# Kernel tuning notes

Measured on AMD Instinct MI355X. Metric: run time of the kernel, lower is better.

## Reference

```python
import jax, jax.numpy as jnp
import numpy as np

PS = 32
D = 256


def setup_inputs() -> dict:
    key = jax.random.key(0)
    ks = jax.random.split(key, 9)
    B, L = 32, 32768
    s_in = 1.0 / np.sqrt(PS)
    s_d = 1.0 / np.sqrt(D)
    return {
        "x": jax.random.normal(ks[0], (B, L), dtype=jnp.float32),
        "W_proj": jax.random.normal(ks[1], (PS, D), dtype=jnp.float32) * s_in,
        "b_proj": jnp.zeros((D,), jnp.float32),
        "W_qkv": jax.random.normal(ks[2], (D, 3 * D), dtype=jnp.float32) * s_d,
        "b_qkv": jnp.zeros((3 * D,), jnp.float32),
        "W_out": jax.random.normal(ks[3], (D, D), dtype=jnp.float32) * s_d,
        "b_out": jnp.zeros((D,), jnp.float32),
        "W_head": jax.random.normal(ks[4], (D, PS), dtype=jnp.float32) * s_d,
        "b_head": jnp.zeros((PS,), jnp.float32),
    }


def reference(x, W_proj, b_proj, W_qkv, b_qkv, W_out, b_out, W_head, b_head):
    B, L = x.shape
    T = L // PS
    # InstanceNorm over full series (torch .std is unbiased -> ddof=1)
    mean = jnp.mean(x, axis=-1, keepdims=True)
    std = jnp.std(x, axis=-1, keepdims=True, ddof=1) + 1e-5
    x_norm = (x - mean) / std
    patches = x_norm.reshape(B, T, PS)
    # Patch embedding
    h = patches @ W_proj + b_proj  # [B, T, D]
    # Single-head causal self-attention (explicit scores, as in source)
    qkv = h @ W_qkv + b_qkv
    q, k, v = jnp.split(qkv, 3, axis=-1)
    scale = 1.0 / jnp.sqrt(jnp.asarray(D, dtype=h.dtype))
    attn = jnp.einsum("btd,bsd->bts", q, k) * scale  # [B, T, T]
    causal = jnp.tril(jnp.ones((T, T), dtype=bool))
    attn = jnp.where(causal, attn, -jnp.inf)
    attn = jax.nn.softmax(attn, axis=-1)
    out = jnp.einsum("bts,bsd->btd", attn, v)
    out = out @ W_out + b_out
    # Prediction head + next-patch MSE loss
    pred = out @ W_head + b_head  # [B, T, PS]
    loss = jnp.mean((pred[:, :-1] - patches[:, 1:]) ** 2)
    return loss
```

## Files before the change

kernel.cpp:

```cpp
#include <hip/hip_runtime.h>
#include <math.h>

#define B_SZ 32
#define L_SZ 32768
#define T_SZ 1024
#define PS_SZ 32
#define D_SZ 256
#define SM_M 10.0f

typedef float f32x4 __attribute__((ext_vector_type(4)));
typedef float f32x16 __attribute__((ext_vector_type(16)));
typedef short s16x8 __attribute__((ext_vector_type(8)));
typedef unsigned short u16x8 __attribute__((ext_vector_type(8)));

__device__ __forceinline__ unsigned short f2bf(float f) {
  union { float f; unsigned int u; } v; v.f = f;
  unsigned int r = v.u + 0x7FFFu + ((v.u >> 16) & 1u);
  return (unsigned short)(r >> 16);
}

__device__ __forceinline__ void g2l16(const unsigned short* g, unsigned short* l) {
  __builtin_amdgcn_global_load_lds(
      (const __attribute__((address_space(1))) unsigned int*)g,
      (__attribute__((address_space(3))) unsigned int*)l, 16, 0, 0);
}

__global__ __launch_bounds__(256) void prep_kernel(const float* __restrict__ x,
                                                   float* __restrict__ sgpart,
                                                   const float* __restrict__ Wp,
                                                   const float* __restrict__ bp,
                                                   const float* __restrict__ Wq,
                                                   const float* __restrict__ bq,
                                                   const float* __restrict__ Wo,
                                                   const float* __restrict__ bo,
                                                   const float* __restrict__ Wh,
                                                   const float* __restrict__ bh,
                                                   float* __restrict__ Wcb,
                                                   unsigned short* __restrict__ WqT,
                                                   unsigned short* __restrict__ WfT,
                                                   float* __restrict__ bfp,
                                                   unsigned int* __restrict__ total,
                                                   float* __restrict__ lsum) {
  __shared__ float red[8];
  const int g = blockIdx.x, tid = threadIdx.x;
  const int w = tid >> 6, lane = tid & 63;
  if (g < 256) {
    const int b = g >> 3;
    const float* p = x + (size_t)b * L_SZ + (size_t)(g & 7) * 4096;
    float s = 0.f, ss = 0.f;
#pragma unroll
    for (int i = 0; i < 4; ++i) {
      float4 f = ((const float4*)p)[tid + i * 256];
      s += f.x + f.y + f.z + f.w;
      ss += f.x * f.x + f.y * f.y + f.z * f.z + f.w * f.w;
    }
#pragma unroll
    for (int off = 32; off >= 1; off >>= 1) {
      s += __shfl_down(s, off);
      ss += __shfl_down(ss, off);
    }
    if (lane == 0) { red[w] = s; red[4 + w] = ss; }
    __syncthreads();
    if (tid == 0) {
      sgpart[g * 2]     = red[0] + red[1] + red[2] + red[3];
      sgpart[g * 2 + 1] = red[4] + red[5] + red[6] + red[7];
    }
  } else if (g < 388) {
    int idx = (g - 256) * 256 + tid;
    if (idx < 33 * 768) {
      int p = idx / 768, j = idx % 768;
      const float* arow = (p < 32) ? (Wp + p * 256) : bp;
      float acc = (p < 32) ? 0.f : bq[j];
      for (int d = 0; d < 256; ++d) acc += arow[d] * Wq[d * 768 + j];
      if (p < 32) WqT[j * 32 + p] = f2bf(acc);
      else Wcb[j] = acc;
    } else {
      int k = idx - 33 * 768;
      if (k < 8192) {
        int p = k >> 8, d = k & 255;
        float acc = 0.f;
        for (int e = 0; e < 256; ++e) acc += Wo[d * 256 + e] * Wh[e * 32 + p];
        WfT[p * 256 + d] = f2bf(acc);
      } else if (k < 8224) {
        int p = k - 8192;
        float acc = bh[p];
        for (int e = 0; e < 256; ++e) acc += bo[e] * Wh[e * 32 + p];
        bfp[p] = acc;
      }
    }
  } else {
    if (tid == 0) { total[0] = 0u; lsum[0] = 0.f; }
  }
}

__global__ __launch_bounds__(256) void qkv_kernel(const float* __restrict__ x,
                                                  const float* __restrict__ sgpart,
                                                  const unsigned short* __restrict__ WqT,
                                                  const float* __restrict__ Wcb,
                                                  unsigned short* __restrict__ Qb,
                                                  unsigned short* __restrict__ Kb,
                                                  unsigned short* __restrict__ Vtt) {
  __shared__ unsigned short T4[4][8448];
  const int tid = threadIdx.x;
  const int w = tid >> 6, lane = tid & 63;
  const int lo = lane & 15, quad = lane >> 4;
  unsigned short* Tw = T4[w];
  const int mbase = blockIdx.x * 128 + w * 32;
  const int b = mbase >> 10;
  float S = 0.f, SS = 0.f;
#pragma unroll
  for (int i = 0; i < 8; ++i) {
    S += sgpart[(b * 8 + i) * 2];
    SS += sgpart[(b * 8 + i) * 2 + 1];
  }
  const float mean = S * (1.f / (float)L_SZ);
  const float var = (SS - S * mean) * (1.f / (float)(L_SZ - 1));
  const float inv = 1.f / (sqrtf(var) + 1e-5f);
  s16x8 af0, af1;
  {
    float4 a = *(const float4*)&x[(size_t)(mbase + lo) * 32 + quad * 8];
    float4 c = *(const float4*)&x[(size_t)(mbase + lo) * 32 + quad * 8 + 4];
    af0[0] = (short)f2bf((a.x - mean) * inv); af0[1] = (short)f2bf((a.y - mean) * inv);
    af0[2] = (short)f2bf((a.z - mean) * inv); af0[3] = (short)f2bf((a.w - mean) * inv);
    af0[4] = (short)f2bf((c.x - mean) * inv); af0[5] = (short)f2bf((c.y - mean) * inv);
    af0[6] = (short)f2bf((c.z - mean) * inv); af0[7] = (short)f2bf((c.w - mean) * inv);
    float4 d = *(const float4*)&x[(size_t)(mbase + 16 + lo) * 32 + quad * 8];
    float4 e = *(const float4*)&x[(size_t)(mbase + 16 + lo) * 32 + quad * 8 + 4];
    af1[0] = (short)f2bf((d.x - mean) * inv); af1[1] = (short)f2bf((d.y - mean) * inv);
    af1[2] = (short)f2bf((d.z - mean) * inv); af1[3] = (short)f2bf((d.w - mean) * inv);
    af1[4] = (short)f2bf((e.x - mean) * inv); af1[5] = (short)f2bf((e.y - mean) * inv);
    af1[6] = (short)f2bf((e.z - mean) * inv); af1[7] = (short)f2bf((e.w - mean) * inv);
  }
#pragma unroll 4
  for (int nt = 0; nt < 16; ++nt) {
    s16x8 bf = *(const s16x8*)&WqT[(size_t)(nt * 16 + lo) * 32 + quad * 8];
    f32x4 c0 = {0.f, 0.f, 0.f, 0.f}, c1 = {0.f, 0.f, 0.f, 0.f};
    c0 = __builtin_amdgcn_mfma_f32_16x16x32_bf16(af0, bf, c0, 0, 0, 0);
    c1 = __builtin_amdgcn_mfma_f32_16x16x32_bf16(af1, bf, c1, 0, 0, 0);
    const int col = nt * 16 + lo;
    const float bi = Wcb[col];
#pragma unroll
    for (int i = 0; i < 4; ++i) {
      Tw[(quad * 4 + i) * 264 + col]      = f2bf((c0[i] + bi) * 0.0625f);
      Tw[(16 + quad * 4 + i) * 264 + col] = f2bf((c1[i] + bi) * 0.0625f);
    }
  }
#pragma unroll
  for (int it = 0; it < 16; ++it) {
    const int gsub = it * 64 + lane;
    const int row = gsub >> 5, c16 = gsub & 31;
    *(u16x8*)&Qb[(size_t)(mbase + row) * 256 + c16 * 8] =
        *(const u16x8*)&Tw[row * 264 + c16 * 8];
  }
#pragma unroll 4
  for (int nt = 0; nt < 16; ++nt) {
    s16x8 bf = *(const s16x8*)&WqT[(size_t)(256 + nt * 16 + lo) * 32 + quad * 8];
    f32x4 c0 = {0.f, 0.f, 0.f, 0.f}, c1 = {0.f, 0.f, 0.f, 0.f};
    c0 = __builtin_amdgcn_mfma_f32_16x16x32_bf16(af0, bf, c0, 0, 0, 0);
    c1 = __builtin_amdgcn_mfma_f32_16x16x32_bf16(af1, bf, c1, 0, 0, 0);
    const int col = nt * 16 + lo;
    const float bi = Wcb[256 + col];
#pragma unroll
    for (int i = 0; i < 4; ++i) {
      Tw[(quad * 4 + i) * 264 + col]      = f2bf(c0[i] + bi);
      Tw[(16 + quad * 4 + i) * 264 + col] = f2bf(c1[i] + bi);
    }
  }
#pragma unroll
  for (int it = 0; it < 16; ++it) {
    const int gsub = it * 64 + lane;
    const int row = gsub >> 5, c16 = gsub & 31;
    *(u16x8*)&Kb[(size_t)(mbase + row) * 256 + c16 * 8] =
        *(const u16x8*)&Tw[row * 264 + c16 * 8];
  }
#pragma unroll 4
  for (int nt2 = 0; nt2 < 16; ++nt2) {
    s16x8 aw = *(const s16x8*)&WqT[(size_t)(512 + nt2 * 16 + lo) * 32 + quad * 8];
    f32x4 c0 = {0.f, 0.f, 0.f, 0.f}, c1 = {0.f, 0.f, 0.f, 0.f};
    c0 = __builtin_amdgcn_mfma_f32_16x16x32_bf16(aw, af0, c0, 0, 0, 0);
    c1 = __builtin_amdgcn_mfma_f32_16x16x32_bf16(aw, af1, c1, 0, 0, 0);
#pragma unroll
    for (int i = 0; i < 4; ++i) {
      const int d = nt2 * 16 + quad * 4 + i;
      const float bv = Wcb[512 + d];
      Tw[d * 32 + lo]      = f2bf(c0[i] + bv);
      Tw[d * 32 + 16 + lo] = f2bf(c1[i] + bv);
    }
  }
  {
    const int ktq = (mbase >> 5) & 31;
    const size_t vb = ((size_t)b * 32 + ktq) * 8192;
#pragma unroll
    for (int it = 0; it < 16; ++it) {
      const int gsub = it * 64 + lane;
      *(u16x8*)&Vtt[vb + gsub * 8] = *(const u16x8*)&Tw[gsub * 8];
    }
  }
}

__global__ __launch_bounds__(128, 1) void attn_kernel(const unsigned short* __restrict__ Qb,
                                                      const unsigned short* __restrict__ Kb,
                                                      const unsigned short* __restrict__ Vtt,
                                                      const unsigned short* __restrict__ WfT,
                                                      const float* __restrict__ bfp,
                                                      const float* __restrict__ x,
                                                      const float* __restrict__ sgpart,
                                                      float* __restrict__ lsum,
                                                      unsigned int* __restrict__ total,
                                                      float* __restrict__ out) {
  __shared__ unsigned short SMEM[36352];
  __shared__ float redf[2];
  __shared__ unsigned int flag;
  const int g = blockIdx.x;
  const int j = g >> 3;
  const int b = (g & 7) * 4 + (j & 3);
  const int qt = (j < 32) ? (15 - (j >> 2)) : ((j - 32) >> 2);
  const int tid = threadIdx.x;
  const int w = tid >> 6, lane = tid & 63;
  const int cl = lane & 31, hi = lane >> 5;
  const int qr0 = qt * 64 + w * 32;

  s16x8 qf[16];
  {
    const size_t qrow = ((size_t)(b * 1024 + qr0 + cl)) * 256;
#pragma unroll
    for (int cb = 0; cb < 16; ++cb)
      qf[cb] = *(const s16x8*)&Qb[qrow + cb * 16 + hi * 8];
  }

  f32x16 O[8], Ol;
#pragma unroll
  for (int dt = 0; dt < 8; ++dt)
#pragma unroll
    for (int i = 0; i < 16; ++i) O[dt][i] = 0.f;
#pragma unroll
  for (int i = 0; i < 16; ++i) Ol[i] = 0.f;
  s16x8 ones;
#pragma unroll
  for (int jj = 0; jj < 8; ++jj) ones[jj] = (short)0x3F80;

  int kof[8];
#pragma unroll
  for (int it = 0; it < 8; ++it) {
    const int key = it * 4 + (tid >> 5);
    kof[it] = key * 256 + ((tid & 31) ^ key) * 8;
  }
  const int vof = (tid >> 2) * 32 + (((tid & 3) ^ ((tid >> 4) & 3))) * 8;
  const unsigned short* KbB = Kb + (size_t)b * 262144;
  const unsigned short* VtB = Vtt + (size_t)b * 262144;
  const int wb = w * 512;
  const int nk = 2 * (qt + 1);

#pragma unroll
  for (int it = 0; it < 8; ++it) g2l16(KbB + kof[it], &SMEM[it * 1024 + wb]);
#pragma unroll
  for (int it = 0; it < 8; ++it) g2l16(VtB + vof + it * 1024, &SMEM[8192 + it * 1024 + wb]);

  const int maskl = (cl >> 2) & 3;
  const int cv0 = (hi ^ maskl) * 8;
  const int cv1 = ((2 | hi) ^ maskl) * 8;
  unsigned short* Pw = &SMEM[32768 + w * 1792];
  const int prow = cl * 56;

  for (int kt = 0; kt < nk; ++kt) {
    const int k0 = kt * 32;
    __syncthreads();
    const int cur = (kt & 1) << 14;
    if (kt + 1 < nk) {
      const int nxt = ((kt + 1) & 1) << 14;
      const int ko = (kt + 1) * 8192;
#pragma unroll
      for (int it = 0; it < 8; ++it) g2l16(KbB + ko + kof[it], &SMEM[nxt + it * 1024 + wb]);
#pragma unroll
      for (int it = 0; it < 8; ++it)
        g2l16(VtB + ko + vof + it * 1024, &SMEM[nxt + 8192 + it * 1024 + wb]);
    }

    if (k0 <= qr0 + 31) {
      f32x16 S;
#pragma unroll
      for (int i = 0; i < 16; ++i) S[i] = 0.f;
      const int kbl = cur + cl * 256;
#pragma unroll
      for (int cb = 0; cb < 16; ++cb) {
        s16x8 kf = *(const s16x8*)&SMEM[kbl + ((((cb << 1) | hi) ^ cl) << 3)];
        S = __builtin_amdgcn_mfma_f32_32x32x16_bf16(qf[cb], kf, S, 0, 0, 0);
      }
      const bool diag = (k0 + 31 > qr0);
#pragma unroll
      for (int r = 0; r < 16; ++r) {
        const int row = (r & 3) + 8 * (r >> 2) + 4 * hi;
        float e = __expf(S[r] - SM_M);
        if (diag && (k0 + cl > qr0 + row)) e = 0.f;
        Pw[row * 56 + cl] = f2bf(e);
      }
      s16x8 pf0 = *(const s16x8*)&Pw[prow + hi * 8];
      s16x8 pf1 = *(const s16x8*)&Pw[prow + 16 + hi * 8];
      Ol = __builtin_amdgcn_mfma_f32_32x32x16_bf16(pf0, ones, Ol, 0, 0, 0);
      Ol = __builtin_amdgcn_mfma_f32_32x32x16_bf16(pf1, ones, Ol, 0, 0, 0);
      const int vbl = cur + 8192 + cl * 32;
#pragma unroll
      for (int dt = 0; dt < 8; ++dt) {
        s16x8 v0 = *(const s16x8*)&SMEM[vbl + dt * 1024 + cv0];
        s16x8 v1 = *(const s16x8*)&SMEM[vbl + dt * 1024 + cv1];
        O[dt] = __builtin_amdgcn_mfma_f32_32x32x16_bf16(pf0, v0, O[dt], 0, 0, 0);
        O[dt] = __builtin_amdgcn_mfma_f32_32x32x16_bf16(pf1, v1, O[dt], 0, 0, 0);
      }
    }
  }
  __syncthreads();

  unsigned short* OLw = &SMEM[w * 8448];
#pragma unroll
  for (int r = 0; r < 16; ++r) {
    const int row = (r & 3) + 8 * (r >> 2) + 4 * hi;
    const float iv = 1.f / Ol[r];
#pragma unroll
    for (int dt = 0; dt < 8; ++dt)
      OLw[row * 264 + dt * 32 + cl] = f2bf(O[dt][r] * iv);
  }
  s16x8 af[16];
#pragma unroll
  for (int cb = 0; cb < 16; ++cb)
    af[cb] = *(const s16x8*)&OLw[cl * 264 + cb * 16 + hi * 8];

  float S_ = 0.f, SS = 0.f;
#pragma unroll
  for (int i = 0; i < 8; ++i) {
    S_ += sgpart[(b * 8 + i) * 2];
    SS += sgpart[(b * 8 + i) * 2 + 1];
  }
  const float mean = S_ * (1.f / (float)L_SZ);
  const float var = (SS - S_ * mean) * (1.f / (float)(L_SZ - 1));
  const float invb = 1.f / (sqrtf(var) + 1e-5f);

  f32x16 hacc;
#pragma unroll
  for (int i = 0; i < 16; ++i) hacc[i] = 0.f;
#pragma unroll
  for (int cb = 0; cb < 16; ++cb) {
    s16x8 bfr = *(const s16x8*)&WfT[(size_t)cl * 256 + cb * 16 + hi * 8];
    hacc = __builtin_amdgcn_mfma_f32_32x32x16_bf16(af[cb], bfr, hacc, 0, 0, 0);
  }
  const float ba = bfp[cl];
  float lacc = 0.f;
#pragma unroll
  for (int r = 0; r < 16; ++r) {
    const int row = (r & 3) + 8 * (r >> 2) + 4 * hi;
    const int t = qr0 + row;
    if (t < 1023) {
      const float pr = hacc[r] + ba;
      const float tg = (x[(size_t)b * L_SZ + (t + 1) * 32 + cl] - mean) * invb;
      const float d = pr - tg;
      lacc += d * d;
    }
  }
#pragma unroll
  for (int off = 32; off >= 1; off >>= 1) lacc += __shfl_down(lacc, off);
  if (lane == 0) redf[w] = lacc;
  __syncthreads();

  if (tid == 0) {
    atomicAdd(lsum, redf[0] + redf[1]);
    __threadfence();
    unsigned int prev = atomicAdd(total, 1u);
    flag = (prev == 511u) ? 1u : 0u;
  }
  __syncthreads();
  if (flag && tid == 0) {
    float tot = atomicAdd(lsum, 0.0f);
    out[0] = tot * (1.f / (float)(B_SZ * (T_SZ - 1) * PS_SZ));
  }
}

extern "C" void kernel_launch(void* const* d_in, const int* in_sizes, int n_in,
                              void* d_out, int out_size, void* d_ws, size_t ws_size,
                              hipStream_t stream) {
  const float* x      = (const float*)d_in[0];
  const float* W_proj = (const float*)d_in[1];
  const float* b_proj = (const float*)d_in[2];
  const float* W_qkv  = (const float*)d_in[3];
  const float* b_qkv  = (const float*)d_in[4];
  const float* W_out  = (const float*)d_in[5];
  const float* b_out  = (const float*)d_in[6];
  const float* W_head = (const float*)d_in[7];
  const float* b_head = (const float*)d_in[8];
  float* out = (float*)d_out;
  char* ws = (char*)d_ws;

  unsigned short* Qb     = (unsigned short*)ws;
  unsigned short* Kb     = (unsigned short*)(ws + (16ull << 20));
  unsigned short* Vtt    = (unsigned short*)(ws + (32ull << 20));
  char* tail = ws + (48ull << 20);
  float*          Wcb    = (float*)tail;
  unsigned short* WqT    = (unsigned short*)(tail + 4096);
  unsigned short* WfT    = (unsigned short*)(tail + 65536);
  float*          bfp    = (float*)(tail + 98304);
  float*          sgpart = (float*)(tail + 102400);
  unsigned int*   total  = (unsigned int*)(tail + 106496);
  float*          lsum   = (float*)(tail + 106496 + 64);

  prep_kernel<<<389, 256, 0, stream>>>(x, sgpart, W_proj, b_proj, W_qkv, b_qkv,
                                       W_out, b_out, W_head, b_head,
                                       Wcb, WqT, WfT, bfp, total, lsum);
  qkv_kernel<<<256, 256, 0, stream>>>(x, sgpart, WqT, Wcb, Qb, Kb, Vtt);
  attn_kernel<<<512, 128, 0, stream>>>(Qb, Kb, Vtt, WfT, bfp, x, sgpart, lsum, total, out);
}
```

Before: 197.1 us.

## Split attention key tiles across four waves with LDS reduction, paired query tiles

Rewrites the attention kernel so each 256-thread block handles two 32-row query tiles (p and 31-p) for load balance. The four waves split the key tiles between them and then combine their partial outputs through an LDS tree reduction. K/V are read directly from global memory instead of being double-buffered into LDS, and P is reshuffled between lanes with cross-half shuffles instead of going through LDS. This aims to raise parallelism and occupancy, at the cost of extra reduction traffic, barriers and uncached global loads per wave.

```diff
diff --git a/kernel.cpp b/kernel.cpp
--- a/kernel.cpp
+++ b/kernel.cpp
@@ -12,17 +12,13 @@
 typedef float f32x16 __attribute__((ext_vector_type(16)));
 typedef short s16x8 __attribute__((ext_vector_type(8)));
 typedef unsigned short u16x8 __attribute__((ext_vector_type(8)));
+typedef unsigned int u32;
+typedef unsigned int u32x4 __attribute__((ext_vector_type(4)));
 
 __device__ __forceinline__ unsigned short f2bf(float f) {
   union { float f; unsigned int u; } v; v.f = f;
   unsigned int r = v.u + 0x7FFFu + ((v.u >> 16) & 1u);
   return (unsigned short)(r >> 16);
-}
-
-__device__ __forceinline__ void g2l16(const unsigned short* g, unsigned short* l) {
-  __builtin_amdgcn_global_load_lds(
-      (const __attribute__((address_space(1))) unsigned int*)g,
-      (__attribute__((address_space(3))) unsigned int*)l, 16, 0, 0);
 }
 
 __global__ __launch_bounds__(256) void prep_kernel(const float* __restrict__ x,
@@ -198,7 +194,7 @@
   }
 }
 
-__global__ __launch_bounds__(128, 1) void attn_kernel(const unsigned short* __restrict__ Qb,
+__global__ __launch_bounds__(256, 2) void attn_kernel(const unsigned short* __restrict__ Qb,
                                                       const unsigned short* __restrict__ Kb,
                                                       const unsigned short* __restrict__ Vtt,
                                                       const unsigned short* __restrict__ WfT,
@@ -208,121 +204,19 @@
                                                       float* __restrict__ lsum,
                                                       unsigned int* __restrict__ total,
                                                       float* __restrict__ out) {
-  __shared__ unsigned short SMEM[36352];
-  __shared__ float redf[2];
-  __shared__ unsigned int flag;
+  __shared__ float CO0[8192];
+  __shared__ float CO1[8192];
+  __shared__ float OlL[4][32];
+  __shared__ unsigned int flagv;
   const int g = blockIdx.x;
-  const int j = g >> 3;
-  const int b = (g & 7) * 4 + (j & 3);
-  const int qt = (j < 32) ? (15 - (j >> 2)) : ((j - 32) >> 2);
+  const int b = (g & 7) * 4 + ((g >> 3) & 3);
+  const int p = g >> 5;
   const int tid = threadIdx.x;
   const int w = tid >> 6, lane = tid & 63;
   const int cl = lane & 31, hi = lane >> 5;
-  const int qr0 = qt * 64 + w * 32;
-
-  s16x8 qf[16];
-  {
-    const size_t qrow = ((size_t)(b * 1024 + qr0 + cl)) * 256;
-#pragma unroll
-    for (int cb = 0; cb < 16; ++cb)
-      qf[cb] = *(const s16x8*)&Qb[qrow + cb * 16 + hi * 8];
-  }
-
-  f32x16 O[8], Ol;
-#pragma unroll
-  for (int dt = 0; dt < 8; ++dt)
-#pragma unroll
-    for (int i = 0; i < 16; ++i) O[dt][i] = 0.f;
-#pragma unroll
-  for (int i = 0; i < 16; ++i) Ol[i] = 0.f;
-  s16x8 ones;
-#pragma unroll
-  for (int jj = 0; jj < 8; ++jj) ones[jj] = (short)0x3F80;
-
-  int kof[8];
-#pragma unroll
-  for (int it = 0; it < 8; ++it) {
-    const int key = it * 4 + (tid >> 5);
-    kof[it] = key * 256 + ((tid & 31) ^ key) * 8;
-  }
-  const int vof = (tid >> 2) * 32 + (((tid & 3) ^ ((tid >> 4) & 3))) * 8;
+
   const unsigned short* KbB = Kb + (size_t)b * 262144;
   const unsigned short* VtB = Vtt + (size_t)b * 262144;
-  const int wb = w * 512;
-  const int nk = 2 * (qt + 1);
-
-#pragma unroll
-  for (int it = 0; it < 8; ++it) g2l16(KbB + kof[it], &SMEM[it * 1024 + wb]);
-#pragma unroll
-  for (int it = 0; it < 8; ++it) g2l16(VtB + vof + it * 1024, &SMEM[8192 + it * 1024 + wb]);
-
-  const int maskl = (cl >> 2) & 3;
-  const int cv0 = (hi ^ maskl) * 8;
-  const int cv1 = ((2 | hi) ^ maskl) * 8;
-  unsigned short* Pw = &SMEM[32768 + w * 1792];
-  const int prow = cl * 56;
-
-  for (int kt = 0; kt < nk; ++kt) {
-    const int k0 = kt * 32;
-    __syncthreads();
-    const int cur = (kt & 1) << 14;
-    if (kt + 1 < nk) {
-      const int nxt = ((kt + 1) & 1) << 14;
-      const int ko = (kt + 1) * 8192;
-#pragma unroll
-      for (int it = 0; it < 8; ++it) g2l16(KbB + ko + kof[it], &SMEM[nxt + it * 1024 + wb]);
-#pragma unroll
-      for (int it = 0; it < 8; ++it)
-        g2l16(VtB + ko + vof + it * 1024, &SMEM[nxt + 8192 + it * 1024 + wb]);
-    }
-
-    if (k0 <= qr0 + 31) {
-      f32x16 S;
-#pragma unroll
-      for (int i = 0; i < 16; ++i) S[i] = 0.f;
-      const int kbl = cur + cl * 256;
-#pragma unroll
-      for (int cb = 0; cb < 16; ++cb) {
-        s16x8 kf = *(const s16x8*)&SMEM[kbl + ((((cb << 1) | hi) ^ cl) << 3)];
-        S = __builtin_amdgcn_mfma_f32_32x32x16_bf16(qf[cb], kf, S, 0, 0, 0);
-      }
-      const bool diag = (k0 + 31 > qr0);
-#pragma unroll
-      for (int r = 0; r < 16; ++r) {
-        const int row = (r & 3) + 8 * (r >> 2) + 4 * hi;
-        float e = __expf(S[r] - SM_M);
-        if (diag && (k0 + cl > qr0 + row)) e = 0.f;
-        Pw[row * 56 + cl] = f2bf(e);
-      }
-      s16x8 pf0 = *(const s16x8*)&Pw[prow + hi * 8];
-      s16x8 pf1 = *(const s16x8*)&Pw[prow + 16 + hi * 8];
-      Ol = __builtin_amdgcn_mfma_f32_32x32x16_bf16(pf0, ones, Ol, 0, 0, 0);
-      Ol = __builtin_amdgcn_mfma_f32_32x32x16_bf16(pf1, ones, Ol, 0, 0, 0);
-      const int vbl = cur + 8192 + cl * 32;
-#pragma unroll
-      for (int dt = 0; dt < 8; ++dt) {
-        s16x8 v0 = *(const s16x8*)&SMEM[vbl + dt * 1024 + cv0];
-        s16x8 v1 = *(const s16x8*)&SMEM[vbl + dt * 1024 + cv1];
-        O[dt] = __builtin_amdgcn_mfma_f32_32x32x16_bf16(pf0, v0, O[dt], 0, 0, 0);
-        O[dt] = __builtin_amdgcn_mfma_f32_32x32x16_bf16(pf1, v1, O[dt], 0, 0, 0);
-      }
-    }
-  }
-  __syncthreads();
-
-  unsigned short* OLw = &SMEM[w * 8448];
-#pragma unroll
-  for (int r = 0; r < 16; ++r) {
-    const int row = (r & 3) + 8 * (r >> 2) + 4 * hi;
-    const float iv = 1.f / Ol[r];
-#pragma unroll
-    for (int dt = 0; dt < 8; ++dt)
-      OLw[row * 264 + dt * 32 + cl] = f2bf(O[dt][r] * iv);
-  }
-  s16x8 af[16];
-#pragma unroll
-  for (int cb = 0; cb < 16; ++cb)
-    af[cb] = *(const s16x8*)&OLw[cl * 264 + cb * 16 + hi * 8];
 
   float S_ = 0.f, SS = 0.f;
 #pragma unroll
@@ -333,41 +227,185 @@
   const float mean = S_ * (1.f / (float)L_SZ);
   const float var = (SS - S_ * mean) * (1.f / (float)(L_SZ - 1));
   const float invb = 1.f / (sqrtf(var) + 1e-5f);
-
-  f32x16 hacc;
-#pragma unroll
-  for (int i = 0; i < 16; ++i) hacc[i] = 0.f;
-#pragma unroll
-  for (int cb = 0; cb < 16; ++cb) {
-    s16x8 bfr = *(const s16x8*)&WfT[(size_t)cl * 256 + cb * 16 + hi * 8];
-    hacc = __builtin_amdgcn_mfma_f32_32x32x16_bf16(af[cb], bfr, hacc, 0, 0, 0);
-  }
-  const float ba = bfp[cl];
   float lacc = 0.f;
-#pragma unroll
-  for (int r = 0; r < 16; ++r) {
-    const int row = (r & 3) + 8 * (r >> 2) + 4 * hi;
-    const int t = qr0 + row;
-    if (t < 1023) {
-      const float pr = hacc[r] + ba;
-      const float tg = (x[(size_t)b * L_SZ + (t + 1) * 32 + cl] - mean) * invb;
-      const float d = pr - tg;
-      lacc += d * d;
-    }
-  }
+
+#pragma unroll 1
+  for (int half = 0; half < 2; ++half) {
+    const int ti = half ? (31 - p) : p;
+    const int qr0 = ti * 32;
+
+    s16x8 qf[16];
+    {
+      const size_t qrow = ((size_t)b * 1024 + qr0 + cl) * 256;
+#pragma unroll
+      for (int cb = 0; cb < 16; ++cb)
+        qf[cb] = *(const s16x8*)&Qb[qrow + cb * 16 + hi * 8];
+    }
+
+    f32x16 O[8];
+#pragma unroll
+    for (int dt = 0; dt < 8; ++dt)
+#pragma unroll
+      for (int i = 0; i < 16; ++i) O[dt][i] = 0.f;
+    float Ol = 0.f;
+
+    for (int kt = w; kt <= ti; kt += 4) {
+      const unsigned short* kp = KbB + (size_t)kt * 8192 + cl * 256 + hi * 8;
+      f32x16 Sx;
+#pragma unroll
+      for (int i = 0; i < 16; ++i) Sx[i] = 0.f;
+#pragma unroll
+      for (int cb = 0; cb < 16; ++cb) {
+        s16x8 kf = *(const s16x8*)&kp[cb * 16];
+        Sx = __builtin_amdgcn_mfma_f32_32x32x16_bf16(kf, qf[cb], Sx, 0, 0, 0);
+      }
+      float e[16];
+      const bool diag = (kt == ti);
+#pragma unroll
+      for (int r = 0; r < 16; ++r) {
+        const int trow = (r & 3) + 8 * (r >> 2) + 4 * hi;
+        float ev = __expf(Sx[r] - SM_M);
+        if (diag && trow > cl) ev = 0.f;
+        e[r] = ev;
+        Ol += ev;
+      }
+      u32 w8[8];
+#pragma unroll
+      for (int m = 0; m < 8; ++m)
+        w8[m] = (u32)f2bf(e[2 * m]) | ((u32)f2bf(e[2 * m + 1]) << 16);
+      const u32 r1 = (u32)__shfl_xor((int)(hi ? w8[0] : w8[2]), 32);
+      const u32 r2 = (u32)__shfl_xor((int)(hi ? w8[1] : w8[3]), 32);
+      const u32 r3 = (u32)__shfl_xor((int)(hi ? w8[4] : w8[6]), 32);
+      const u32 r4 = (u32)__shfl_xor((int)(hi ? w8[5] : w8[7]), 32);
+      union { u32x4 u; s16x8 s; } p0, p1;
+      p0.u[0] = hi ? r1 : w8[0];
+      p0.u[1] = hi ? r2 : w8[1];
+      p0.u[2] = hi ? w8[2] : r1;
+      p0.u[3] = hi ? w8[3] : r2;
+      p1.u[0] = hi ? r3 : w8[4];
+      p1.u[1] = hi ? r4 : w8[5];
+      p1.u[2] = hi ? w8[6] : r3;
+      p1.u[3] = hi ? w8[7] : r4;
+      const unsigned short* vp = VtB + (size_t)kt * 8192 + cl * 32 + hi * 8;
+#pragma unroll
+      for (int dt = 0; dt < 8; ++dt) {
+        s16x8 v0 = *(const s16x8*)&vp[dt * 1024];
+        s16x8 v1 = *(const s16x8*)&vp[dt * 1024 + 16];
+        O[dt] = __builtin_amdgcn_mfma_f32_32x32x16_bf16(p0.s, v0, O[dt], 0, 0, 0);
+        O[dt] = __builtin_amdgcn_mfma_f32_32x32x16_bf16(p1.s, v1, O[dt], 0, 0, 0);
+      }
+    }
+    Ol += __shfl_xor(Ol, 32);
+
+    __syncthreads();
+    if (w == 1) {
+#pragma unroll
+      for (int dt = 0; dt < 8; ++dt)
+#pragma unroll
+        for (int r = 0; r < 16; ++r) {
+          const int row = (r & 3) + 8 * (r >> 2) + 4 * hi;
+          CO0[row * 256 + dt * 32 + cl] = O[dt][r];
+        }
+    }
+    if (w == 3) {
+#pragma unroll
+      for (int dt = 0; dt < 8; ++dt)
+#pragma unroll
+        for (int r = 0; r < 16; ++r) {
+          const int row = (r & 3) + 8 * (r >> 2) + 4 * hi;
+          CO1[row * 256 + dt * 32 + cl] = O[dt][r];
+        }
+    }
+    if (hi == 0) OlL[w][cl] = Ol;
+    __syncthreads();
+    if (w == 0) {
+#pragma unroll
+      for (int dt = 0; dt < 8; ++dt)
+#pragma unroll
+        for (int r = 0; r < 16; ++r) {
+          const int row = (r & 3) + 8 * (r >> 2) + 4 * hi;
+          O[dt][r] += CO0[row * 256 + dt * 32 + cl];
+        }
+    }
+    if (w == 2) {
+#pragma unroll
+      for (int dt = 0; dt < 8; ++dt)
+#pragma unroll
+        for (int r = 0; r < 16; ++r) {
+          const int row = (r & 3) + 8 * (r >> 2) + 4 * hi;
+          O[dt][r] += CO1[row * 256 + dt * 32 + cl];
+        }
+    }
+    __syncthreads();
+    if (w == 2) {
+#pragma unroll
+      for (int dt = 0; dt < 8; ++dt)
+#pragma unroll
+        for (int r = 0; r < 16; ++r) {
+          const int row = (r & 3) + 8 * (r >> 2) + 4 * hi;
+          CO0[row * 256 + dt * 32 + cl] = O[dt][r];
+        }
+    }
+    __syncthreads();
+    if (w == 0) {
+#pragma unroll
+      for (int dt = 0; dt < 8; ++dt)
+#pragma unroll
+        for (int r = 0; r < 16; ++r) {
+          const int row = (r & 3) + 8 * (r >> 2) + 4 * hi;
+          O[dt][r] += CO0[row * 256 + dt * 32 + cl];
+        }
+      float ivr[16];
+#pragma unroll
+      for (int r = 0; r < 16; ++r) {
+        const int row = (r & 3) + 8 * (r >> 2) + 4 * hi;
+        ivr[r] = 1.f / (OlL[0][row] + OlL[1][row] + OlL[2][row] + OlL[3][row]);
+      }
+      unsigned short* OLw = (unsigned short*)CO0;
+#pragma unroll
+      for (int dt = 0; dt < 8; ++dt)
+#pragma unroll
+        for (int r = 0; r < 16; ++r) {
+          const int row = (r & 3) + 8 * (r >> 2) + 4 * hi;
+          OLw[row * 264 + dt * 32 + cl] = f2bf(O[dt][r] * ivr[r]);
+        }
+      s16x8 af[16];
+#pragma unroll
+      for (int cb = 0; cb < 16; ++cb)
+        af[cb] = *(const s16x8*)&OLw[cl * 264 + cb * 16 + hi * 8];
+      f32x16 hacc;
+#pragma unroll
+      for (int i = 0; i < 16; ++i) hacc[i] = 0.f;
+#pragma unroll
+      for (int cb = 0; cb < 16; ++cb) {
+        s16x8 bfr = *(const s16x8*)&WfT[(size_t)cl * 256 + cb * 16 + hi * 8];
+        hacc = __builtin_amdgcn_mfma_f32_32x32x16_bf16(af[cb], bfr, hacc, 0, 0, 0);
+      }
+      const float ba = bfp[cl];
+#pragma unroll
+      for (int r = 0; r < 16; ++r) {
+        const int row = (r & 3) + 8 * (r >> 2) + 4 * hi;
+        const int t = qr0 + row;
+        if (t < 1023) {
+          const float pr = hacc[r] + ba;
+          const float tg = (x[(size_t)b * L_SZ + (t + 1) * 32 + cl] - mean) * invb;
+          const float d = pr - tg;
+          lacc += d * d;
+        }
+      }
+    }
+  }
+
 #pragma unroll
   for (int off = 32; off >= 1; off >>= 1) lacc += __shfl_down(lacc, off);
-  if (lane == 0) redf[w] = lacc;
-  __syncthreads();
-
   if (tid == 0) {
-    atomicAdd(lsum, redf[0] + redf[1]);
+    atomicAdd(lsum, lacc);
     __threadfence();
     unsigned int prev = atomicAdd(total, 1u);
-    flag = (prev == 511u) ? 1u : 0u;
+    flagv = (prev == 511u) ? 1u : 0u;
   }
   __syncthreads();
-  if (flag && tid == 0) {
+  if (flagv && tid == 0) {
     float tot = atomicAdd(lsum, 0.0f);
     out[0] = tot * (1.f / (float)(B_SZ * (T_SZ - 1) * PS_SZ));
   }
@@ -404,5 +442,5 @@
                                        W_out, b_out, W_head, b_head,
                                        Wcb, WqT, WfT, bfp, total, lsum);
   qkv_kernel<<<256, 256, 0, stream>>>(x, sgpart, WqT, Wcb, Qb, Kb, Vtt);
-  attn_kernel<<<512, 128, 0, stream>>>(Qb, Kb, Vtt, WfT, bfp, x, sgpart, lsum, total, out);
+  attn_kernel<<<512, 256, 0, stream>>>(Qb, Kb, Vtt, WfT, bfp, x, sgpart, lsum, total, out);
 }
```

Result: no change. 196.9 us (-0.1%).
